# Performance work log

Measured on AMD Instinct MI355X. Metric: run time of the kernel, lower is better.

The kernel has to match this reference:

```python
import jax, jax.numpy as jnp
import numpy as np

NUM_HEADS = 16

def setup_inputs() -> dict:
    key = jax.random.key(0)
    ks = jax.random.split(key, 9)
    B, N, D = 4, 4096, 1024
    s = 1.0 / np.sqrt(D)
    return {
        "x": jax.random.normal(ks[0], (B, N, D), dtype=jnp.float32),
        "Wq": jax.random.normal(ks[1], (D, D), dtype=jnp.float32) * s,
        "bq": jnp.zeros((D,), dtype=jnp.float32),
        "Wk": jax.random.normal(ks[2], (D, D), dtype=jnp.float32) * s,
        "bk": jnp.zeros((D,), dtype=jnp.float32),
        "Wv": jax.random.normal(ks[3], (D, D), dtype=jnp.float32) * s,
        "bv": jnp.zeros((D,), dtype=jnp.float32),
        "Wp": jax.random.normal(ks[4], (D, D), dtype=jnp.float32) * s,
        "bp": jnp.zeros((D,), dtype=jnp.float32),
    }

def _split_heads(t, H):
    B, N, D = t.shape
    return t.reshape(B, N, H, D // H).transpose(0, 2, 1, 3)  # [B,H,N,hd]

def reference(x, Wq, bq, Wk, bk, Wv, bv, Wp, bp):
    H = NUM_HEADS
    q = jax.nn.elu(x @ Wq + bq) + 1.0   # elu feature map (config.elu=True)
    k = jax.nn.elu(x @ Wk + bk) + 1.0
    v = x @ Wv + bv
    q, k, v = _split_heads(q, H), _split_heads(k, H), _split_heads(v, H)
    # k^T v: [B,H,hd,hd]
    kv = jnp.einsum('bhnd,bhne->bhde', k, v)
    numerator = jnp.einsum('bhnd,bhde->bhne', q, kv)  # [B,H,N,hd]
    # adaptive normalizer: q @ sum_k
    sum_k = k.sum(axis=2)  # [B,H,hd]
    denominator = jnp.einsum('bhnd,bhd->bhn', q, sum_k)[..., None]
    y = numerator / denominator
    B, _, N, hd = y.shape
    y = y.transpose(0, 2, 1, 3).reshape(B, N, H * hd)
    return y @ Wp + bp
```

## Files before the change

kernel.cpp:

```cpp
#include <hip/hip_runtime.h>
#include <hip/hip_bf16.h>

typedef __attribute__((ext_vector_type(4))) float f32x4;
typedef __attribute__((ext_vector_type(4))) short s16x4;
typedef __attribute__((ext_vector_type(8))) short s16x8;
typedef __attribute__((ext_vector_type(8))) __bf16 bf16x8;

#define DEV static __device__ __forceinline__

DEV float bf2f(ushort u){
  unsigned x = ((unsigned)u) << 16;
  return __builtin_bit_cast(float, x);
}
DEV ushort f2bf(float f){
  unsigned x = __builtin_bit_cast(unsigned, f);
  x += 0x7fffu + ((x >> 16) & 1u);
  return (ushort)(x >> 16);
}
DEV void load_lds16(const void* g, void* l){
  __builtin_amdgcn_global_load_lds((const __attribute__((address_space(1))) void*)g,
                                   (__attribute__((address_space(3))) void*)l, 16, 0, 0);
}

__global__ __launch_bounds__(256) void k_cvt_x(const float* __restrict__ x,
                                               ushort* __restrict__ xb, int n8){
  int i = blockIdx.x * 256 + threadIdx.x;
  if (i >= n8) return;
  const f32x4* p = (const f32x4*)(x + (size_t)i * 8);
  f32x4 a = p[0], b = p[1];
  s16x8 o;
  o[0]=(short)f2bf(a[0]); o[1]=(short)f2bf(a[1]); o[2]=(short)f2bf(a[2]); o[3]=(short)f2bf(a[3]);
  o[4]=(short)f2bf(b[0]); o[5]=(short)f2bf(b[1]); o[6]=(short)f2bf(b[2]); o[7]=(short)f2bf(b[3]);
  *(s16x8*)(xb + (size_t)i * 8) = o;
}

__global__ void k_transposeW(const float* __restrict__ Wq, const float* __restrict__ Wk,
                             const float* __restrict__ Wv, const float* __restrict__ Wp,
                             ushort* __restrict__ qkvT, ushort* __restrict__ wpT){
  __shared__ float tile[32][33];
  int z = blockIdx.z;
  const float* W = (z == 0) ? Wq : (z == 1) ? Wk : (z == 2) ? Wv : Wp;
  ushort* out = (z < 3) ? (qkvT + (size_t)z * 1024 * 1024) : wpT;
  int bx = blockIdx.x * 32, by = blockIdx.y * 32;
  int tx = threadIdx.x, ty = threadIdx.y;
  #pragma unroll
  for (int j = 0; j < 32; j += 8)
    tile[ty + j][tx] = W[(size_t)(by + ty + j) * 1024 + bx + tx];
  __syncthreads();
  #pragma unroll
  for (int j = 0; j < 32; j += 8)
    out[(size_t)(bx + ty + j) * 1024 + by + tx] = f2bf(tile[tx][ty + j]);
}

template<int MODE>
__global__ __launch_bounds__(512, 1) void k_gemm(
    const ushort* __restrict__ A, const ushort* __restrict__ Bt,
    const float* __restrict__ b0, const float* __restrict__ b1, const float* __restrict__ b2,
    ushort* __restrict__ oQ, ushort* __restrict__ oK, ushort* __restrict__ oV,
    float* __restrict__ oF, int N)
{
  const int K = 1024;
  const int NT = 16;
  __shared__ ushort ldsA[2][16384];
  __shared__ ushort ldsB[2][16384];

  int wg = blockIdx.x;
  int cpx = gridDim.x >> 3;
  wg = (wg & 7) * cpx + (wg >> 3);
  int nbn = N >> 8;
  int bmi = wg / nbn, bni = wg - bmi * nbn;
  int m0 = bmi << 8, n0 = bni << 8;
  int tid = threadIdx.x, wid = tid >> 6, lane = tid & 63;
  int wr = wid >> 2, wc = wid & 3;
  int hi = lane >> 4, L = lane & 15;

  int rr = tid >> 3;
  int gaA = ((tid & 7) ^ (rr & 7)) << 3;
  int gaB = ((tid & 7) ^ ((tid >> 5) & 7)) << 3;
  const ushort* gA = A  + (size_t)(m0 + rr) * K + gaA;
  const ushort* gB = Bt + (size_t)(n0 + rr) * K + gaB;
  int ldst = wid << 10;

  int swz = (hi ^ (L & 7)) << 4;
  int arow = (wr * 128 + L) << 7;
  int brow = ((wc * 64 + L * 4)) << 7;

  f32x4 acc[8][4] = {};
  bf16x8 aX[4], aY[4], bX[4], bY[4];

  #define RD_A(SET, BASE, MH, KX)                                              \
    _Pragma("unroll")                                                          \
    for (int m = 0; m < 4; ++m)                                                \
      SET[m] = *(const bf16x8*)((BASE) + arow + (MH) * 8192 + (m << 11) + (swz ^ (KX)));
  #define RD_B(SET, BASE, KX)                                                  \
    _Pragma("unroll")                                                          \
    for (int n = 0; n < 4; ++n)                                                \
      SET[n] = *(const bf16x8*)((BASE) + brow + (n << 7) + (swz ^ (KX)));
  #define MF(MOFF, ASET, BSET)                                                 \
    __builtin_amdgcn_s_setprio(1);                                             \
    _Pragma("unroll")                                                          \
    for (int m = 0; m < 4; ++m)                                                \
      _Pragma("unroll")                                                        \
      for (int n = 0; n < 4; ++n)                                              \
        acc[m + (MOFF)][n] =                                                   \
          __builtin_amdgcn_mfma_f32_16x16x32_bf16(ASET[m], BSET[n], acc[m + (MOFF)][n], 0, 0, 0); \
    __builtin_amdgcn_s_setprio(0);

  #define ST_B0(SB, kof) load_lds16(gB + (kof),                   (SB) + ldst);
  #define ST_B1(SB, kof) load_lds16(gB + (size_t) 64 * K + (kof), (SB) + 8192  + ldst);
  #define ST_B2(SB, kof) load_lds16(gB + (size_t)128 * K + (kof), (SB) + 16384 + ldst);
  #define ST_B3(SB, kof) load_lds16(gB + (size_t)192 * K + (kof), (SB) + 24576 + ldst);
  #define ST_A0(SA, kof) load_lds16(gA + (kof),                   (SA) + ldst);
  #define ST_A2(SA, kof) load_lds16(gA + (size_t)128 * K + (kof), (SA) + 16384 + ldst);
  #define ST_A1(SA, kof) load_lds16(gA + (size_t) 64 * K + (kof), (SA) + 8192  + ldst);
  #define ST_A3(SA, kof) load_lds16(gA + (size_t)192 * K + (kof), (SA) + 24576 + ldst);

  {
    char* SA0 = (char*)&ldsA[0][0];
    char* SB0 = (char*)&ldsB[0][0];
    char* SB1 = (char*)&ldsB[1][0];
    ST_B0(SB0, 0) ST_B1(SB0, 0) ST_B2(SB0, 0) ST_B3(SB0, 0)
    ST_A0(SA0, 0) ST_A2(SA0, 0) ST_A1(SA0, 0) ST_A3(SA0, 0)
    ST_B0(SB1, 64) ST_B1(SB1, 64)
  }
  asm volatile("s_waitcnt vmcnt(4)" ::: "memory");
  __builtin_amdgcn_s_barrier();
  RD_A(aX, (const char*)&ldsA[0][0], 0, 0)
  RD_B(bX, (const char*)&ldsB[0][0], 0)

  int buf = 0;
  for (int t = 0; t < NT; ++t) {
    const char* LA = (const char*)&ldsA[buf][0];
    const char* LB = (const char*)&ldsB[buf][0];
    char* SAn = (char*)&ldsA[buf ^ 1][0];
    char* SBn = (char*)&ldsB[buf ^ 1][0];
    char* SBc = (char*)&ldsB[buf][0];
    size_t k1 = (size_t)(t + 1) << 6;
    size_t k2 = (size_t)(t + 2) << 6;
    bool st1 = (t + 1) < NT, st2 = (t + 2) < NT;

    if (st1) asm volatile("s_waitcnt vmcnt(2)" ::: "memory");
    else     asm volatile("s_waitcnt vmcnt(0)" ::: "memory");
    __builtin_amdgcn_s_barrier();
    RD_A(aY, LA, 1, 0)
    if (st1) { ST_B2(SBn, k1) ST_B3(SBn, k1) }
    __builtin_amdgcn_sched_barrier(0);
    MF(0, aX, bX)

    __builtin_amdgcn_s_barrier();
    RD_A(aX, LA, 1, 64)
    RD_B(bY, LB, 64)
    if (st1) { ST_A0(SAn, k1) ST_A2(SAn, k1) }
    __builtin_amdgcn_sched_barrier(0);
    MF(4, aY, bX)

    __builtin_amdgcn_s_barrier();
    RD_A(aY, LA, 0, 64)
    if (st1) { ST_A1(SAn, k1) ST_A3(SAn, k1) }
    __builtin_amdgcn_sched_barrier(0);
    MF(4, aX, bY)

    asm volatile("s_waitcnt vmcnt(2)" ::: "memory");
    __builtin_amdgcn_s_barrier();
    if (st1) { RD_A(aX, SAn, 0, 0) RD_B(bX, SBn, 0) }
    if (st2) { ST_B0(SBc, k2) ST_B1(SBc, k2) }
    __builtin_amdgcn_sched_barrier(0);
    MF(0, aY, bY)

    buf ^= 1;
  }
  #undef RD_A
  #undef RD_B
  #undef MF

  int row0 = m0 + wr * 128 + (hi << 2);
  int cb4 = n0 + wc * 64 + (L << 2);
  if constexpr (MODE == 0) {
    f32x4 bias; ushort* dst; bool act;
    if (cb4 < 1024)      { bias = *(const f32x4*)(b0 + cb4);          dst = oQ + cb4;          act = true;  }
    else if (cb4 < 2048) { bias = *(const f32x4*)(b1 + (cb4 - 1024)); dst = oK + (cb4 - 1024); act = true;  }
    else                 { bias = *(const f32x4*)(b2 + (cb4 - 2048)); dst = oV + (cb4 - 2048); act = false; }
    #pragma unroll
    for (int m = 0; m < 8; ++m)
      #pragma unroll
      for (int j = 0; j < 4; ++j) {
        int r = row0 + m * 16 + j;
        s16x4 w;
        #pragma unroll
        for (int n = 0; n < 4; ++n) {
          float v = acc[m][n][j] + bias[n];
          if (act) v = (v > 0.f) ? (v + 1.f) : __expf(v);
          w[n] = (short)f2bf(v);
        }
        *(s16x4*)(dst + (size_t)r * 1024) = w;
      }
  } else {
    f32x4 bias = *(const f32x4*)(b0 + cb4);
    #pragma unroll
    for (int m = 0; m < 8; ++m)
      #pragma unroll
      for (int j = 0; j < 4; ++j) {
        int r = row0 + m * 16 + j;
        f32x4 w;
        #pragma unroll
        for (int n = 0; n < 4; ++n) w[n] = acc[m][n][j] + bias[n];
        *(f32x4*)(oF + (size_t)r * 1024 + cb4) = w;
      }
  }
}

__global__ __launch_bounds__(256, 2) void k_kv(
    const ushort* __restrict__ kbuf, const ushort* __restrict__ vbuf,
    float* __restrict__ kvp, float* __restrict__ skp)
{
  __shared__ ushort tile[2][8192];
  __shared__ float red[64 * 68];
  __shared__ float skred[4][64];

  int bh = blockIdx.x >> 3, chunk = blockIdx.x & 7;
  int b = bh >> 4, h = bh & 15;
  int tid = threadIdx.x, wid = tid >> 6, lane = tid & 63;
  int d0 = (lane >> 3) << 3, e0 = (lane & 7) << 3;

  size_t gbase = ((size_t)b * 4096 + chunk * 512 + wid * 16 + (lane >> 3)) * 1024
               + h * 64 + (lane & 7) * 8;

  float acc[8][8] = {};
  float sk[8] = {};

  #define STAGE_KV(bp, c)                                                     \
  { char* base_ = (char*)&tile[bp][0] + (wid << 11);                          \
    size_t g_ = gbase + (size_t)(c) * 65536;                                  \
    load_lds16(kbuf + g_,        base_);                                      \
    load_lds16(kbuf + g_ + 8192, base_ + 1024);                               \
    load_lds16(vbuf + g_,        base_ + 8192);                               \
    load_lds16(vbuf + g_ + 8192, base_ + 9216); }

  STAGE_KV(0, 0)

  for (int c = 0; c < 8; ++c) {
    if (c + 1 < 8) {
      STAGE_KV((c + 1) & 1, c + 1)
      asm volatile("s_waitcnt vmcnt(4)" ::: "memory");
    } else {
      asm volatile("s_waitcnt vmcnt(0)" ::: "memory");
    }
    __builtin_amdgcn_s_barrier();
    const ushort* Ks = &tile[c & 1][0];
    const ushort* Vs = &tile[c & 1][4096];
    #pragma unroll
    for (int t = 0; t < 16; ++t) {
      int nn = (wid << 4) + t;
      s16x8 k8 = *(const s16x8*)(Ks + nn * 64 + d0);
      s16x8 v8 = *(const s16x8*)(Vs + nn * 64 + e0);
      float kf[8], vf[8];
      #pragma unroll
      for (int i = 0; i < 8; ++i) { kf[i] = bf2f((ushort)k8[i]); vf[i] = bf2f((ushort)v8[i]); }
      #pragma unroll
      for (int i = 0; i < 8; ++i) {
        sk[i] += kf[i];
        #pragma unroll
        for (int j = 0; j < 8; ++j) acc[i][j] += kf[i] * vf[j];
      }
    }
    __builtin_amdgcn_sched_barrier(0);
    __builtin_amdgcn_s_barrier();
  }
  #undef STAGE_KV

  for (int w = 0; w < 4; ++w) {
    if (wid == w) {
      #pragma unroll
      for (int i = 0; i < 8; ++i)
        #pragma unroll
        for (int j4 = 0; j4 < 2; ++j4) {
          f32x4 v4;
          v4[0] = acc[i][j4 * 4 + 0]; v4[1] = acc[i][j4 * 4 + 1];
          v4[2] = acc[i][j4 * 4 + 2]; v4[3] = acc[i][j4 * 4 + 3];
          float* p = &red[(d0 + i) * 68 + e0 + j4 * 4];
          if (w == 0) *(f32x4*)p = v4;
          else        { f32x4 o = *(const f32x4*)p; *(f32x4*)p = o + v4; }
        }
    }
    __syncthreads();
  }

  size_t kvbase = ((size_t)chunk * 64 + bh) * 4096;
  #pragma unroll
  for (int i = 0; i < 16; ++i) {
    int el = tid + i * 256;
    kvp[kvbase + el] = red[(el >> 6) * 68 + (el & 63)];
  }
  if ((lane & 7) == 0) {
    #pragma unroll
    for (int i = 0; i < 8; ++i) skred[wid][d0 + i] = sk[i];
  }
  __syncthreads();
  if (tid < 64) {
    float s = 0.f;
    #pragma unroll
    for (int w = 0; w < 4; ++w) s += skred[w][tid];
    skp[(((size_t)chunk * 64 + bh) << 6) + tid] = s;
  }
}

__global__ __launch_bounds__(512, 2) void k_num(
    const ushort* __restrict__ qbuf, const float* __restrict__ kvp,
    const float* __restrict__ skp, ushort* __restrict__ ybuf)
{
  __shared__ float kvf[4096];
  __shared__ ushort kvtb[4096];
  __shared__ ushort skb[64];

  int bh = blockIdx.x >> 3, chunk = blockIdx.x & 7;
  int b = bh >> 4, h = bh & 15;
  int tid = threadIdx.x, wid = tid >> 6, lane = tid & 63;
  int hi = lane >> 4, L = lane & 15;

  #pragma unroll
  for (int i = 0; i < 2; ++i) {
    int i4 = tid + i * 512;
    f32x4 s = {0.f, 0.f, 0.f, 0.f};
    #pragma unroll
    for (int sl = 0; sl < 8; ++sl)
      s += *(const f32x4*)&kvp[(((size_t)sl * 64 + bh) << 12) + ((size_t)i4 << 2)];
    *(f32x4*)&kvf[i4 << 2] = s;
  }
  if (tid < 64) {
    float s = 0.f;
    #pragma unroll
    for (int sl = 0; sl < 8; ++sl) s += skp[(((size_t)sl * 64 + bh) << 6) + tid];
    skb[tid] = f2bf(s);
  }
  __syncthreads();
  {
    int e = tid >> 3, dg = tid & 7;
    s16x8 o;
    #pragma unroll
    for (int j = 0; j < 8; ++j) o[j] = (short)f2bf(kvf[(dg * 8 + j) * 64 + e]);
    *(s16x8*)((char*)kvtb + e * 128 + ((dg ^ (e & 7)) << 4)) = o;
  }
  __syncthreads();

  size_t r0 = (size_t)b * 4096 + chunk * 512 + wid * 64;
  const ushort* qb = qbuf + (r0 + L) * 1024 + h * 64 + hi * 8;

  f32x4 acc[4][4] = {};
  f32x4 accd[4] = {};
  #pragma unroll
  for (int kk = 0; kk < 2; ++kk) {
    bf16x8 bfr[4], bfd;
    bfd = *(const bf16x8*)((const char*)skb + kk * 64 + hi * 16);
    #pragma unroll
    for (int n = 0; n < 4; ++n) {
      int e = L * 4 + n;
      bfr[n] = *(const bf16x8*)((char*)kvtb + e * 128 + ((((kk << 2) | hi) ^ (e & 7)) << 4));
    }
    #pragma unroll
    for (int m = 0; m < 4; ++m) {
      bf16x8 af = *(const bf16x8*)(qb + (size_t)m * 16 * 1024 + kk * 32);
      #pragma unroll
      for (int n = 0; n < 4; ++n)
        acc[m][n] = __builtin_amdgcn_mfma_f32_16x16x32_bf16(af, bfr[n], acc[m][n], 0, 0, 0);
      accd[m] = __builtin_amdgcn_mfma_f32_16x16x32_bf16(af, bfd, accd[m], 0, 0, 0);
    }
  }

  #pragma unroll
  for (int m = 0; m < 4; ++m)
    #pragma unroll
    for (int j = 0; j < 4; ++j) {
      float inv = 1.0f / accd[m][j];
      s16x4 w;
      #pragma unroll
      for (int n = 0; n < 4; ++n) w[n] = (short)f2bf(acc[m][n][j] * inv);
      *(s16x4*)(ybuf + (r0 + m * 16 + hi * 4 + j) * 1024 + h * 64 + L * 4) = w;
    }
}

extern "C" void kernel_launch(void* const* d_in, const int* in_sizes, int n_in,
                              void* d_out, int out_size, void* d_ws, size_t ws_size,
                              hipStream_t stream)
{
  const float* x  = (const float*)d_in[0];
  const float* Wq = (const float*)d_in[1];
  const float* bq = (const float*)d_in[2];
  const float* Wk = (const float*)d_in[3];
  const float* bk = (const float*)d_in[4];
  const float* Wv = (const float*)d_in[5];
  const float* bv = (const float*)d_in[6];
  const float* Wp = (const float*)d_in[7];
  const float* bp = (const float*)d_in[8];

  char* ws = (char*)d_ws;
  ushort* xb    = (ushort*)(ws + 0);
  ushort* qkvT  = (ushort*)(ws + 33554432);
  ushort* wpT   = (ushort*)(ws + 39845888);
  ushort* ybuf  = (ushort*)(ws + 41943040);
  float*  kvp   = (float*)(ws + 0);
  float*  skp   = (float*)(ws + 8388608);

  ushort* vbuf = (ushort*)d_out;
  ushort* qbuf = (ushort*)d_out + 16777216;
  ushort* kbuf = ybuf;

  k_cvt_x<<<8192, 256, 0, stream>>>(x, xb, 2097152);
  k_transposeW<<<dim3(32, 32, 4), dim3(32, 8), 0, stream>>>(Wq, Wk, Wv, Wp, qkvT, wpT);
  k_gemm<0><<<768, 512, 0, stream>>>(xb, qkvT, bq, bk, bv, qbuf, kbuf, vbuf, nullptr, 3072);
  k_kv<<<512, 256, 0, stream>>>(kbuf, vbuf, kvp, skp);
  k_num<<<512, 512, 0, stream>>>(qbuf, kvp, skp, ybuf);
  k_gemm<1><<<256, 512, 0, stream>>>(ybuf, wpT, bp, nullptr, nullptr,
                                     nullptr, nullptr, nullptr, (float*)d_out, 1024);
}
```

Baseline: 236.9 us.

## Merge prep kernels and restructure GEMM main loop into 8-phase pipeline

```diff
diff --git a/kernel.cpp b/kernel.cpp
--- a/kernel.cpp
+++ b/kernel.cpp
@@ -22,34 +22,37 @@
                                    (__attribute__((address_space(3))) void*)l, 16, 0, 0);
 }
 
-__global__ __launch_bounds__(256) void k_cvt_x(const float* __restrict__ x,
-                                               ushort* __restrict__ xb, int n8){
-  int i = blockIdx.x * 256 + threadIdx.x;
-  if (i >= n8) return;
-  const f32x4* p = (const f32x4*)(x + (size_t)i * 8);
-  f32x4 a = p[0], b = p[1];
-  s16x8 o;
-  o[0]=(short)f2bf(a[0]); o[1]=(short)f2bf(a[1]); o[2]=(short)f2bf(a[2]); o[3]=(short)f2bf(a[3]);
-  o[4]=(short)f2bf(b[0]); o[5]=(short)f2bf(b[1]); o[6]=(short)f2bf(b[2]); o[7]=(short)f2bf(b[3]);
-  *(s16x8*)(xb + (size_t)i * 8) = o;
-}
-
-__global__ void k_transposeW(const float* __restrict__ Wq, const float* __restrict__ Wk,
-                             const float* __restrict__ Wv, const float* __restrict__ Wp,
-                             ushort* __restrict__ qkvT, ushort* __restrict__ wpT){
+__global__ __launch_bounds__(256) void k_prep(
+    const float* __restrict__ x, ushort* __restrict__ xb,
+    const float* __restrict__ Wq, const float* __restrict__ Wk,
+    const float* __restrict__ Wv, const float* __restrict__ Wp,
+    ushort* __restrict__ qkvT, ushort* __restrict__ wpT)
+{
   __shared__ float tile[32][33];
-  int z = blockIdx.z;
-  const float* W = (z == 0) ? Wq : (z == 1) ? Wk : (z == 2) ? Wv : Wp;
-  ushort* out = (z < 3) ? (qkvT + (size_t)z * 1024 * 1024) : wpT;
-  int bx = blockIdx.x * 32, by = blockIdx.y * 32;
-  int tx = threadIdx.x, ty = threadIdx.y;
-  #pragma unroll
-  for (int j = 0; j < 32; j += 8)
-    tile[ty + j][tx] = W[(size_t)(by + ty + j) * 1024 + bx + tx];
-  __syncthreads();
-  #pragma unroll
-  for (int j = 0; j < 32; j += 8)
-    out[(size_t)(bx + ty + j) * 1024 + by + tx] = f2bf(tile[tx][ty + j]);
+  int bid = blockIdx.x, tid = threadIdx.x;
+  if (bid < 8192) {
+    int i = bid * 256 + tid;
+    const f32x4* p = (const f32x4*)(x + (size_t)i * 8);
+    f32x4 a = p[0], b = p[1];
+    s16x8 o;
+    o[0]=(short)f2bf(a[0]); o[1]=(short)f2bf(a[1]); o[2]=(short)f2bf(a[2]); o[3]=(short)f2bf(a[3]);
+    o[4]=(short)f2bf(b[0]); o[5]=(short)f2bf(b[1]); o[6]=(short)f2bf(b[2]); o[7]=(short)f2bf(b[3]);
+    *(s16x8*)(xb + (size_t)i * 8) = o;
+  } else {
+    int r = bid - 8192;
+    int z = r >> 10; r &= 1023;
+    const float* W = (z == 0) ? Wq : (z == 1) ? Wk : (z == 2) ? Wv : Wp;
+    ushort* out = (z < 3) ? (qkvT + (size_t)z * 1024 * 1024) : wpT;
+    int bx = (r & 31) * 32, by = (r >> 5) * 32;
+    int tx = tid & 31, ty = tid >> 5;
+    #pragma unroll
+    for (int j = 0; j < 32; j += 8)
+      tile[ty + j][tx] = W[(size_t)(by + ty + j) * 1024 + bx + tx];
+    __syncthreads();
+    #pragma unroll
+    for (int j = 0; j < 32; j += 8)
+      out[(size_t)(bx + ty + j) * 1024 + by + tx] = f2bf(tile[tx][ty + j]);
+  }
 }
 
 template<int MODE>
@@ -60,7 +63,6 @@
     float* __restrict__ oF, int N)
 {
   const int K = 1024;
-  const int NT = 16;
   __shared__ ushort ldsA[2][16384];
   __shared__ ushort ldsB[2][16384];
 
@@ -86,92 +88,89 @@
   int brow = ((wc * 64 + L * 4)) << 7;
 
   f32x4 acc[8][4] = {};
-  bf16x8 aX[4], aY[4], bX[4], bY[4];
-
-  #define RD_A(SET, BASE, MH, KX)                                              \
+  bf16x8 af[4], bf[4];
+
+  #define RD_A(BASE, MH, KX)                                                   \
     _Pragma("unroll")                                                          \
     for (int m = 0; m < 4; ++m)                                                \
-      SET[m] = *(const bf16x8*)((BASE) + arow + (MH) * 8192 + (m << 11) + (swz ^ (KX)));
-  #define RD_B(SET, BASE, KX)                                                  \
+      af[m] = *(const bf16x8*)((BASE) + arow + (MH) * 8192 + (m << 11) + (swz ^ (KX)));
+  #define RD_B(BASE, KX)                                                       \
     _Pragma("unroll")                                                          \
     for (int n = 0; n < 4; ++n)                                                \
-      SET[n] = *(const bf16x8*)((BASE) + brow + (n << 7) + (swz ^ (KX)));
-  #define MF(MOFF, ASET, BSET)                                                 \
-    __builtin_amdgcn_s_setprio(1);                                             \
+      bf[n] = *(const bf16x8*)((BASE) + brow + (n << 7) + (swz ^ (KX)));
+  #define MFMA16(MOFF)                                                         \
     _Pragma("unroll")                                                          \
     for (int m = 0; m < 4; ++m)                                                \
       _Pragma("unroll")                                                        \
       for (int n = 0; n < 4; ++n)                                              \
         acc[m + (MOFF)][n] =                                                   \
-          __builtin_amdgcn_mfma_f32_16x16x32_bf16(ASET[m], BSET[n], acc[m + (MOFF)][n], 0, 0, 0); \
-    __builtin_amdgcn_s_setprio(0);
-
-  #define ST_B0(SB, kof) load_lds16(gB + (kof),                   (SB) + ldst);
-  #define ST_B1(SB, kof) load_lds16(gB + (size_t) 64 * K + (kof), (SB) + 8192  + ldst);
-  #define ST_B2(SB, kof) load_lds16(gB + (size_t)128 * K + (kof), (SB) + 16384 + ldst);
-  #define ST_B3(SB, kof) load_lds16(gB + (size_t)192 * K + (kof), (SB) + 24576 + ldst);
-  #define ST_A0(SA, kof) load_lds16(gA + (kof),                   (SA) + ldst);
-  #define ST_A2(SA, kof) load_lds16(gA + (size_t)128 * K + (kof), (SA) + 16384 + ldst);
-  #define ST_A1(SA, kof) load_lds16(gA + (size_t) 64 * K + (kof), (SA) + 8192  + ldst);
-  #define ST_A3(SA, kof) load_lds16(gA + (size_t)192 * K + (kof), (SA) + 24576 + ldst);
-
+          __builtin_amdgcn_mfma_f32_16x16x32_bf16(af[m], bf[n], acc[m + (MOFF)][n], 0, 0, 0);
+
+  #define ST_A0(SA_, kof) load_lds16(gA + (kof),                   (SA_) + ldst);
+  #define ST_A1(SA_, kof) load_lds16(gA + (size_t) 64 * K + (kof), (SA_) + 8192  + ldst);
+  #define ST_A2(SA_, kof) load_lds16(gA + (size_t)128 * K + (kof), (SA_) + 16384 + ldst);
+  #define ST_A3(SA_, kof) load_lds16(gA + (size_t)192 * K + (kof), (SA_) + 24576 + ldst);
+  #define ST_B0(SB_, kof) load_lds16(gB + (kof),                   (SB_) + ldst);
+  #define ST_B1(SB_, kof) load_lds16(gB + (size_t) 64 * K + (kof), (SB_) + 8192  + ldst);
+  #define ST_B2(SB_, kof) load_lds16(gB + (size_t)128 * K + (kof), (SB_) + 16384 + ldst);
+  #define ST_B3(SB_, kof) load_lds16(gB + (size_t)192 * K + (kof), (SB_) + 24576 + ldst);
+
+  #define PH8(LA_, LB_, MH, KX, MOFF, STG, WAIT)                               \
+  { STG                                                                        \
+    WAIT                                                                       \
+    RD_A(LA_, MH, KX)                                                          \
+    RD_B(LB_, KX)                                                              \
+    asm volatile("s_waitcnt lgkmcnt(0)" ::: "memory");                         \
+    __builtin_amdgcn_sched_barrier(0);                                         \
+    __builtin_amdgcn_s_setprio(1);                                             \
+    MFMA16(MOFF)                                                               \
+    __builtin_amdgcn_s_setprio(0);                                             \
+    __builtin_amdgcn_s_barrier(); }
+
+  #define W2 { asm volatile("s_waitcnt vmcnt(2)" ::: "memory"); __builtin_amdgcn_s_barrier(); }
+  #define W0 { asm volatile("s_waitcnt vmcnt(0)" ::: "memory"); __builtin_amdgcn_s_barrier(); }
+
+  char* SA0 = (char*)&ldsA[0][0];
+  char* SA1 = (char*)&ldsA[1][0];
+  char* SB0 = (char*)&ldsB[0][0];
+  char* SB1 = (char*)&ldsB[1][0];
+  const char* LA0 = (const char*)&ldsA[0][0];
+  const char* LA1 = (const char*)&ldsA[1][0];
+  const char* LB0 = (const char*)&ldsB[0][0];
+  const char* LB1 = (const char*)&ldsB[1][0];
+
+  ST_A0(SA0, 0) ST_A1(SA0, 0) ST_A2(SA0, 0) ST_A3(SA0, 0)
+  ST_B0(SB0, 0) ST_B1(SB0, 0) ST_B2(SB0, 0) ST_B3(SB0, 0)
+
+  for (int i = 0; i < 7; ++i) {
+    size_t ko  = (size_t)(2 * i + 1) << 6;
+    size_t ke2 = (size_t)(2 * i + 2) << 6;
+    PH8(LA0, LB0, 0, 0,  0, { ST_A1(SA1, ko) ST_A3(SA1, ko) }, W2)
+    PH8(LA0, LB0, 0, 64, 0, { ST_A0(SA1, ko) ST_A2(SA1, ko) }, )
+    PH8(LA0, LB0, 1, 64, 4, { ST_B0(SB1, ko) ST_B1(SB1, ko) }, )
+    PH8(LA0, LB0, 1, 0,  4, { ST_B2(SB1, ko) ST_B3(SB1, ko) }, )
+    PH8(LA1, LB1, 0, 0,  0, { ST_A1(SA0, ke2) ST_A3(SA0, ke2) }, W2)
+    PH8(LA1, LB1, 0, 64, 0, { ST_A0(SA0, ke2) ST_A2(SA0, ke2) }, )
+    PH8(LA1, LB1, 1, 64, 4, { ST_B0(SB0, ke2) ST_B1(SB0, ke2) }, )
+    PH8(LA1, LB1, 1, 0,  4, { ST_B2(SB0, ke2) ST_B3(SB0, ke2) }, )
+  }
   {
-    char* SA0 = (char*)&ldsA[0][0];
-    char* SB0 = (char*)&ldsB[0][0];
-    char* SB1 = (char*)&ldsB[1][0];
-    ST_B0(SB0, 0) ST_B1(SB0, 0) ST_B2(SB0, 0) ST_B3(SB0, 0)
-    ST_A0(SA0, 0) ST_A2(SA0, 0) ST_A1(SA0, 0) ST_A3(SA0, 0)
-    ST_B0(SB1, 64) ST_B1(SB1, 64)
-  }
-  asm volatile("s_waitcnt vmcnt(4)" ::: "memory");
-  __builtin_amdgcn_s_barrier();
-  RD_A(aX, (const char*)&ldsA[0][0], 0, 0)
-  RD_B(bX, (const char*)&ldsB[0][0], 0)
-
-  int buf = 0;
-  for (int t = 0; t < NT; ++t) {
-    const char* LA = (const char*)&ldsA[buf][0];
-    const char* LB = (const char*)&ldsB[buf][0];
-    char* SAn = (char*)&ldsA[buf ^ 1][0];
-    char* SBn = (char*)&ldsB[buf ^ 1][0];
-    char* SBc = (char*)&ldsB[buf][0];
-    size_t k1 = (size_t)(t + 1) << 6;
-    size_t k2 = (size_t)(t + 2) << 6;
-    bool st1 = (t + 1) < NT, st2 = (t + 2) < NT;
-
-    if (st1) asm volatile("s_waitcnt vmcnt(2)" ::: "memory");
-    else     asm volatile("s_waitcnt vmcnt(0)" ::: "memory");
-    __builtin_amdgcn_s_barrier();
-    RD_A(aY, LA, 1, 0)
-    if (st1) { ST_B2(SBn, k1) ST_B3(SBn, k1) }
-    __builtin_amdgcn_sched_barrier(0);
-    MF(0, aX, bX)
-
-    __builtin_amdgcn_s_barrier();
-    RD_A(aX, LA, 1, 64)
-    RD_B(bY, LB, 64)
-    if (st1) { ST_A0(SAn, k1) ST_A2(SAn, k1) }
-    __builtin_amdgcn_sched_barrier(0);
-    MF(4, aY, bX)
-
-    __builtin_amdgcn_s_barrier();
-    RD_A(aY, LA, 0, 64)
-    if (st1) { ST_A1(SAn, k1) ST_A3(SAn, k1) }
-    __builtin_amdgcn_sched_barrier(0);
-    MF(4, aX, bY)
-
-    asm volatile("s_waitcnt vmcnt(2)" ::: "memory");
-    __builtin_amdgcn_s_barrier();
-    if (st1) { RD_A(aX, SAn, 0, 0) RD_B(bX, SBn, 0) }
-    if (st2) { ST_B0(SBc, k2) ST_B1(SBc, k2) }
-    __builtin_amdgcn_sched_barrier(0);
-    MF(0, aY, bY)
-
-    buf ^= 1;
-  }
+    size_t ko = (size_t)15 << 6;
+    PH8(LA0, LB0, 0, 0,  0, { ST_A1(SA1, ko) ST_A3(SA1, ko) }, W2)
+    PH8(LA0, LB0, 0, 64, 0, { ST_A0(SA1, ko) ST_A2(SA1, ko) }, )
+    PH8(LA0, LB0, 1, 64, 4, { ST_B0(SB1, ko) ST_B1(SB1, ko) }, )
+    PH8(LA0, LB0, 1, 0,  4, { ST_B2(SB1, ko) ST_B3(SB1, ko) }, )
+    PH8(LA1, LB1, 0, 0,  0, { }, W0)
+    PH8(LA1, LB1, 0, 64, 0, { }, )
+    PH8(LA1, LB1, 1, 64, 4, { }, )
+    PH8(LA1, LB1, 1, 0,  4, { }, )
+  }
+  #undef PH8
+  #undef W2
+  #undef W0
   #undef RD_A
   #undef RD_B
-  #undef MF
+  #undef MFMA16
 
   int row0 = m0 + wr * 128 + (hi << 2);
   int cb4 = n0 + wc * 64 + (L << 2);
@@ -404,8 +403,7 @@
   ushort* qbuf = (ushort*)d_out + 16777216;
   ushort* kbuf = ybuf;
 
-  k_cvt_x<<<8192, 256, 0, stream>>>(x, xb, 2097152);
-  k_transposeW<<<dim3(32, 32, 4), dim3(32, 8), 0, stream>>>(Wq, Wk, Wv, Wp, qkvT, wpT);
+  k_prep<<<12288, 256, 0, stream>>>(x, xb, Wq, Wk, Wv, Wp, qkvT, wpT);
   k_gemm<0><<<768, 512, 0, stream>>>(xb, qkvT, bq, bk, bv, qbuf, kbuf, vbuf, nullptr, 3072);
   k_kv<<<512, 256, 0, stream>>>(kbuf, vbuf, kvp, skp);
   k_num<<<512, 512, 0, stream>>>(qbuf, kvp, skp, ybuf);
```

New measurement: 265.6 us. 12.1% more time.
